# Optimization experiments

Measured on AMD Instinct MI355X. Metric: run time of the kernel, lower is better.

## Reference

```python
import jax, jax.numpy as jnp
import numpy as np

DIM = 128; NH = 4; WS = 7; SS = 3
ZP, HP, WP = 14, 56, 56
NMLP = 512; EPS = 1e-5
N = WS ** 3  # tokens per window (343)


def _ln(x, g, b):
    m = x.mean(-1, keepdims=True)
    v = x.var(-1, keepdims=True)
    return (x - m) / jnp.sqrt(v + EPS) * g + b


def _rel_index():
    # static relative-position index for a cubic (WS,WS,WS) window
    c = np.stack(np.meshgrid(np.arange(WS), np.arange(WS), np.arange(WS), indexing='ij')).reshape(3, -1)
    rel = (c[:, :, None] - c[:, None, :]).transpose(1, 2, 0) + (WS - 1)
    rel[..., 0] *= (2 * WS - 1) ** 2
    rel[..., 1] *= (2 * WS - 1)
    return rel.sum(-1).reshape(-1)  # [N*N]


def _attn_mask():
    # static shifted-window attention mask, [nW, N, N]
    img = np.zeros((ZP, HP, WP), np.float32)
    cnt = 0
    sl = (slice(0, -WS), slice(-WS, -SS), slice(-SS, None))
    for z in sl:
        for h in sl:
            for w in sl:
                img[z, h, w] = cnt
                cnt += 1
    m = img.reshape(ZP // WS, WS, HP // WS, WS, WP // WS, WS)
    m = m.transpose(0, 2, 4, 1, 3, 5).reshape(-1, N)
    d = m[:, None, :] - m[:, :, None]
    return np.where(d != 0, np.float32(-100.0), np.float32(0.0))


_REL_IDX = jnp.asarray(_rel_index())
_MASK = jnp.asarray(_attn_mask())


def setup_inputs() -> dict:
    key = jax.random.key(0)
    ks = jax.random.split(key, 8)
    return {
        'x': jax.random.normal(ks[0], (2, ZP, HP, WP, DIM), jnp.float32),
        'norm1_g': jnp.ones((DIM,), jnp.float32),
        'norm1_b': jnp.zeros((DIM,), jnp.float32),
        'qkv_w': jax.random.normal(ks[1], (DIM, 3 * DIM), jnp.float32) * 0.02,
        'qkv_b': jnp.zeros((3 * DIM,), jnp.float32),
        'rel_table': jax.random.normal(ks[2], ((2 * WS - 1) ** 3, NH), jnp.float32) * 0.02,
        'proj_w': jax.random.normal(ks[3], (DIM, DIM), jnp.float32) * 0.02,
        'proj_b': jnp.zeros((DIM,), jnp.float32),
        'norm2_g': jnp.ones((DIM,), jnp.float32),
        'norm2_b': jnp.zeros((DIM,), jnp.float32),
        'fc1_w': jax.random.normal(ks[4], (DIM, NMLP), jnp.float32) * 0.02,
        'fc1_b': jnp.zeros((NMLP,), jnp.float32),
        'fc2_w': jax.random.normal(ks[5], (NMLP, DIM), jnp.float32) * 0.02,
        'fc2_b': jnp.zeros((DIM,), jnp.float32),
    }


def reference(x, norm1_g, norm1_b, qkv_w, qkv_b, rel_table, proj_w, proj_b,
              norm2_g, norm2_b, fc1_w, fc1_b, fc2_w, fc2_b):
    B, Z, H, W, C = x.shape
    hd = C // NH
    scale = hd ** -0.5
    shortcut = x
    xn = _ln(x, norm1_g, norm1_b)
    # cyclic shift
    xs = jnp.roll(xn, (-SS, -SS, -SS), axis=(1, 2, 3))
    # window partition -> [B*nW, N, C]
    xw = xs.reshape(B, Z // WS, WS, H // WS, WS, W // WS, WS, C)
    xw = xw.transpose(0, 1, 3, 5, 2, 4, 6, 7).reshape(-1, N, C)
    qkv = (xw @ qkv_w + qkv_b).reshape(-1, N, 3, NH, hd).transpose(2, 0, 3, 1, 4)
    q, k, v = qkv[0], qkv[1], qkv[2]  # [Bn, NH, N, hd]
    attn = jnp.einsum('bhnd,bhmd->bhnm', q * scale, k)
    bias = rel_table[_REL_IDX].reshape(N, N, NH).transpose(2, 0, 1)  # [NH, N, N]
    attn = attn + bias[None]
    nW = _MASK.shape[0]
    attn = attn.reshape(B, nW, NH, N, N) + _MASK[None, :, None]
    attn = jax.nn.softmax(attn.reshape(-1, NH, N, N), axis=-1)
    out = jnp.einsum('bhnm,bhmd->bhnd', attn, v)
    out = out.transpose(0, 2, 1, 3).reshape(-1, N, C)
    out = out @ proj_w + proj_b
    # window reverse -> [B, Z, H, W, C]
    out = out.reshape(B, Z // WS, H // WS, W // WS, WS, WS, WS, C)
    out = out.transpose(0, 1, 4, 2, 5, 3, 6, 7).reshape(B, Z, H, W, C)
    out = jnp.roll(out, (SS, SS, SS), axis=(1, 2, 3))
    x1 = shortcut + out
    y = _ln(x1, norm2_g, norm2_b)
    y = jax.nn.gelu(y @ fc1_w + fc1_b, approximate=False) @ fc2_w + fc2_b
    return x1 + y
```

## Files before the change

### kernel.cpp

```cpp
#include <hip/hip_runtime.h>


typedef __attribute__((ext_vector_type(8))) _Float16 half8;
typedef __attribute__((ext_vector_type(4))) _Float16 half4;
typedef __attribute__((ext_vector_type(4))) float floatx4;

#define DEV static __device__ __forceinline__

DEV floatx4 MFMA(half8 a, half8 b, floatx4 c) {
  return __builtin_amdgcn_mfma_f32_16x16x32_f16(a, b, c, 0, 0, 0);
}
DEV floatx4 MFMA16(half4 a, half4 b, floatx4 c) {
  return __builtin_amdgcn_mfma_f32_16x16x16f16(a, b, c, 0, 0, 0);
}

DEV float gelu_f(float v) {
  return v / (1.f + __expf(-1.702f * v));
}

DEV void f4arr(float4 v, float o[4]) {
  o[0] = v.x; o[1] = v.y; o[2] = v.z; o[3] = v.w;
}

DEV void stage_load(half8 pf[8], const _Float16* src, int rst, int tid) {
#pragma unroll
  for (int it = 0; it < 8; ++it) {
    int e = it * 256 + tid;
    int row = e >> 4, seg = e & 15;
    pf[it] = *(const half8*)&src[(size_t)row * rst + seg * 8];
  }
}
DEV void stage_store(_Float16* wb, const half8 pf[8], int tid) {
#pragma unroll
  for (int it = 0; it < 8; ++it) {
    int e = it * 256 + tid;
    int row = e >> 4, seg = e & 15;
    *(half8*)&wb[row * 136 + seg * 8] = pf[it];
  }
}
DEV void stage_tile(_Float16* wb, const _Float16* src, int rst, int tid) {
  half8 pf[8];
  stage_load(pf, src, rst, tid);
  stage_store(wb, pf, tid);
}

__global__ __launch_bounds__(256) void k_prep(
    const float* __restrict__ rel, _Float16* __restrict__ biasH,
    const float* __restrict__ w1, const float* __restrict__ w2,
    const float* __restrict__ wq, const float* __restrict__ wp,
    _Float16* __restrict__ w1h, _Float16* __restrict__ w2h,
    _Float16* __restrict__ wqh, _Float16* __restrict__ wph) {
  int gid = blockIdx.x * 256 + threadIdx.x;
  if (gid < 495616) {
    int reg = gid & 3, quad = (gid >> 2) & 3, ml = (gid >> 4) & 15;
    int u = gid >> 8;
    int nt = u % 22; u /= 22;
    int rt = u % 22; int h = u / 22;
    int q = rt * 16 + ml, kv = nt * 16 + quad * 4 + reg;
    float val = -30000.f;
    if (q < 343 && kv < 343) {
      int lzi = q / 49, ri = q - lzi * 49, lhi = ri / 7, lwi = ri - lhi * 7;
      int lzj = kv / 49, rj = kv - lzj * 49, lhj = rj / 7, lwj = rj - lhj * 7;
      int idx = (lzi - lzj + 6) * 169 + (lhi - lhj + 6) * 13 + (lwi - lwj + 6);
      val = rel[idx * 4 + h];
    }
    biasH[gid] = (_Float16)val;
    return;
  }
  int i = gid - 495616;
  if (i < 65536) {
    int n = i >> 7, k = i & 127;
    w1h[i] = (_Float16)w1[k * 512 + n];
  } else if (i < 131072) {
    int j = i - 65536; int n = j >> 9, k = j & 511;
    w2h[j] = (_Float16)w2[k * 128 + n];
  } else if (i < 180224) {
    int j = i - 131072; int n = j >> 7, k = j & 127;
    wqh[j] = (_Float16)wq[k * 384 + n];
  } else if (i < 196608) {
    int j = i - 180224; int n = j >> 7, k = j & 127;
    wph[j] = (_Float16)wp[k * 128 + n];
  }
}

__global__ __launch_bounds__(256) void k_ln_qkv(
    const float* __restrict__ x, const float* __restrict__ g1,
    const float* __restrict__ b1, const _Float16* __restrict__ wqh,
    const float* __restrict__ bq, _Float16* __restrict__ qkv) {
  __shared__ __align__(16) _Float16 wb[128 * 136];
  const int tid = threadIdx.x, lane = tid & 63, wid = tid >> 6;
  const int ml = lane & 15, quad = lane >> 4;
  const int task = blockIdx.x * 4 + wid;
  const int w = task / 11, pr = task - (task / 11) * 11;
  const int b_ = w >> 7, r = w & 127;
  const int wz = r >> 6, wh = (r >> 3) & 7, ww = r & 7;

  half8 a0[4], a1[4];
#pragma unroll
  for (int hf = 0; hf < 2; ++hf) {
    int t = pr * 32 + hf * 16 + ml; if (t > 342) t = 342;
    int lz = t / 49, rr = t - lz * 49, lh = rr / 7, lw = rr - lh * 7;
    int oz = wz * 7 + lz + 3; if (oz >= 14) oz -= 14;
    int oh = wh * 7 + lh + 3; if (oh >= 56) oh -= 56;
    int ow = ww * 7 + lw + 3; if (ow >= 56) ow -= 56;
    const float* xp = x + ((((b_ * 14 + oz) * 56 + oh) * 56 + ow) << 7);
    float xv[32];
    float s = 0.f, ss = 0.f;
#pragma unroll
    for (int ks = 0; ks < 4; ++ks) {
      float4 p0 = *(const float4*)(xp + ks * 32 + quad * 8);
      float4 p1 = *(const float4*)(xp + ks * 32 + quad * 8 + 4);
      xv[ks * 8 + 0] = p0.x; xv[ks * 8 + 1] = p0.y; xv[ks * 8 + 2] = p0.z; xv[ks * 8 + 3] = p0.w;
      xv[ks * 8 + 4] = p1.x; xv[ks * 8 + 5] = p1.y; xv[ks * 8 + 6] = p1.z; xv[ks * 8 + 7] = p1.w;
      s += (p0.x + p0.y) + (p0.z + p0.w) + (p1.x + p1.y) + (p1.z + p1.w);
      ss += (p0.x * p0.x + p0.y * p0.y) + (p0.z * p0.z + p0.w * p0.w) +
            (p1.x * p1.x + p1.y * p1.y) + (p1.z * p1.z + p1.w * p1.w);
    }
    s += __shfl_xor(s, 16); s += __shfl_xor(s, 32);
    ss += __shfl_xor(ss, 16); ss += __shfl_xor(ss, 32);
    float mean = s * 0.0078125f;
    float rstd = rsqrtf(ss * 0.0078125f - mean * mean + 1e-5f);
#pragma unroll
    for (int ks = 0; ks < 4; ++ks) {
      int k0 = ks * 32 + quad * 8;
      float4 gg0 = *(const float4*)(g1 + k0), gg1 = *(const float4*)(g1 + k0 + 4);
      float4 bb0 = *(const float4*)(b1 + k0), bb1 = *(const float4*)(b1 + k0 + 4);
      half8 a;
      a[0] = (_Float16)((xv[ks * 8 + 0] - mean) * rstd * gg0.x + bb0.x);
      a[1] = (_Float16)((xv[ks * 8 + 1] - mean) * rstd * gg0.y + bb0.y);
      a[2] = (_Float16)((xv[ks * 8 + 2] - mean) * rstd * gg0.z + bb0.z);
      a[3] = (_Float16)((xv[ks * 8 + 3] - mean) * rstd * gg0.w + bb0.w);
      a[4] = (_Float16)((xv[ks * 8 + 4] - mean) * rstd * gg1.x + bb1.x);
      a[5] = (_Float16)((xv[ks * 8 + 5] - mean) * rstd * gg1.y + bb1.y);
      a[6] = (_Float16)((xv[ks * 8 + 6] - mean) * rstd * gg1.z + bb1.z);
      a[7] = (_Float16)((xv[ks * 8 + 7] - mean) * rstd * gg1.w + bb1.w);
      if (hf == 0) a0[ks] = a; else a1[ks] = a;
    }
  }

  const int t0 = pr * 32 + ml;
  const int t1 = t0 + 16;
  _Float16* q0 = qkv + ((size_t)w * 343 + t0) * 384;
  _Float16* q1 = qkv + ((size_t)w * 343 + (t1 < 343 ? t1 : 342)) * 384;

  for (int c = 0; c < 3; ++c) {
    __syncthreads();
    stage_tile(wb, wqh + (size_t)c * 128 * 128, 128, tid);
    __syncthreads();
    for (int ntl = 0; ntl < 8; ++ntl) {
      floatx4 acc0 = {0.f, 0.f, 0.f, 0.f}, acc1 = {0.f, 0.f, 0.f, 0.f};
#pragma unroll
      for (int ks = 0; ks < 4; ++ks) {
        half8 bb = *(const half8*)&wb[(ntl * 16 + ml) * 136 + ks * 32 + quad * 8];
        acc0 = MFMA(bb, a0[ks], acc0);
        acc1 = MFMA(bb, a1[ks], acc1);
      }
      const int colb = c * 128 + ntl * 16 + quad * 4;
      float qb[4]; f4arr(*(const float4*)&bq[colb], qb);
      half4 s0, s1;
#pragma unroll
      for (int reg = 0; reg < 4; ++reg) {
        s0[reg] = (_Float16)(acc0[reg] + qb[reg]);
        s1[reg] = (_Float16)(acc1[reg] + qb[reg]);
      }
      *(half4*)&q0[colb] = s0;
      if (t1 < 343) *(half4*)&q1[colb] = s1;
    }
  }
}

__global__ __launch_bounds__(512, 2) void k_attn(const _Float16* __restrict__ qkv,
                                                 const _Float16* __restrict__ biasH,
                                                 _Float16* __restrict__ aout) {
  __shared__ __align__(16) _Float16 kl[352 * 40];
  __shared__ __align__(16) _Float16 vt[32 * 364];
  __shared__ __align__(16) _Float16 pen[27 * 360];
  __shared__ __align__(4) unsigned char region[352];
  const int tid = threadIdx.x;
  const int w = blockIdx.x >> 2, head = blockIdx.x & 3;
  const int r = w & 127;
  const int wz = r >> 6, wh = (r >> 3) & 7, ww = r & 7;
  const bool fz = (wz == 1), fh = (wh == 7), fw = (ww == 7);

  for (int t = tid; t < 352; t += 512) {
    int rg = 255;
    if (t < 343) {
      int lz = t / 49, rr = t - lz * 49, lh = rr / 7, lw = rr - lh * 7;
      int rz = fz ? (lz < 4 ? 1 : 2) : 0;
      int rh2 = fh ? (lh < 4 ? 1 : 2) : 0;
      int rw2 = fw ? (lw < 4 ? 1 : 2) : 0;
      rg = rz * 9 + rh2 * 3 + rw2;
    }
    region[t] = (unsigned char)rg;
  }
  for (int e = tid; e < 27 * 352; e += 512) {
    int rg = e / 352, t = e - rg * 352;
    int rt_ = 255;
    if (t < 343) {
      int lz = t / 49, rr = t - lz * 49, lh = rr / 7, lw = rr - lh * 7;
      int rz = fz ? (lz < 4 ? 1 : 2) : 0;
      int rh2 = fh ? (lh < 4 ? 1 : 2) : 0;
      int rw2 = fw ? (lw < 4 ? 1 : 2) : 0;
      rt_ = rz * 9 + rh2 * 3 + rw2;
    }
    pen[rg * 360 + t] = (rt_ == rg) ? (_Float16)0.f : (_Float16)(-30000.f);
  }
  const _Float16* qkvw = qkv + (size_t)w * 343 * 384;
  for (int e = tid; e < 352 * 4; e += 512) {
    int t = e >> 2, d8 = (e & 3) * 8;
    half8 v;
    if (t < 343) {
      v = *(const half8*)&qkvw[t * 384 + 128 + head * 32 + d8];
    } else {
#pragma unroll
      for (int j = 0; j < 8; ++j) v[j] = (_Float16)0.f;
    }
    *(half8*)&kl[t * 40 + d8] = v;
  }
  for (int e = tid; e < 343 * 4; e += 512) {
    int t = e >> 2, d8 = (e & 3) * 8;
    half8 v = *(const half8*)&qkvw[t * 384 + 256 + head * 32 + d8];
#pragma unroll
    for (int j = 0; j < 8; ++j) vt[(d8 + j) * 364 + t] = v[j];
  }
  for (int e = tid; e < 9 * 32; e += 512) {
    int t = 343 + (e >> 5), d = e & 31;
    vt[d * 364 + t] = (_Float16)0.f;
  }
  __syncthreads();

  const int lane = tid & 63, wid = tid >> 6;
  const int ml = lane & 15, quad = lane >> 4;
  const float scale = 0.17677669529663687f;

  for (int rt = wid; rt < 22; rt += 8) {
    const int row0 = rt * 16;
    int qrow = row0 + ml; if (qrow > 342) qrow = 342;
    half8 bq8 = *(const half8*)&qkvw[qrow * 384 + head * 32 + quad * 8];
    const int rq = region[qrow];
    const _Float16* penr = &pen[rq * 360 + quad * 4];
    const _Float16* bb = &biasH[(size_t)((head * 22 + rt) * 22) * 256 + ml * 16 + quad * 4];

    floatx4 o0 = {0.f, 0.f, 0.f, 0.f}, o1 = {0.f, 0.f, 0.f, 0.f};
    floatx4 sm4 = {0.f, 0.f, 0.f, 0.f};
#pragma unroll
    for (int g = 0; g < 3; ++g) {
      const int G = (g < 2) ? 8 : 6;
      const int nb = g * 8;
      half4 bp[8];
      floatx4 S[8];
#pragma unroll
      for (int k = 0; k < 8; ++k) if (k < G) {
        half4 b4 = *(const half4*)&bb[(nb + k) * 256];
        half4 p4 = *(const half4*)&penr[(nb + k) * 16];
        bp[k] = b4 + p4;
      }
#pragma unroll
      for (int k = 0; k < 8; ++k) if (k < G) {
        half8 ak = *(const half8*)&kl[((nb + k) * 16 + ml) * 40 + quad * 8];
        S[k] = MFMA(ak, bq8, (floatx4){0.f, 0.f, 0.f, 0.f});
      }
#pragma unroll
      for (int k = 0; k < 8; ++k) if (k < G) {
        half4 p;
#pragma unroll
        for (int reg = 0; reg < 4; ++reg) {
          float v = fmaf(S[k][reg], scale, (float)bp[k][reg]);
          float e = __expf(v);
          sm4[reg] += e;
          p[reg] = (_Float16)e;
        }
        half4 va0 = *(const half4*)&vt[ml * 364 + (nb + k) * 16 + quad * 4];
        half4 va1 = *(const half4*)&vt[(16 + ml) * 364 + (nb + k) * 16 + quad * 4];
        o0 = MFMA16(va0, p, o0);
        o1 = MFMA16(va1, p, o1);
      }
    }
    float sm = (sm4[0] + sm4[1]) + (sm4[2] + sm4[3]);
    sm += __shfl_xor(sm, 16);
    sm += __shfl_xor(sm, 32);

    const int orow = row0 + ml;
    if (orow < 343) {
      float inv = 1.f / sm;
      _Float16* op = aout + ((size_t)w * 343 + orow) * 128 + head * 32;
      half4 s0, s1;
#pragma unroll
      for (int reg = 0; reg < 4; ++reg) {
        s0[reg] = (_Float16)(o0[reg] * inv);
        s1[reg] = (_Float16)(o1[reg] * inv);
      }
      *(half4*)&op[quad * 4] = s0;
      *(half4*)&op[16 + quad * 4] = s1;
    }
  }
}

__global__ __launch_bounds__(256, 2) void k_pm(
    const _Float16* __restrict__ aout, const _Float16* __restrict__ wph,
    const float* __restrict__ bp, const float* __restrict__ x,
    const float* __restrict__ g2, const float* __restrict__ nb2,
    const _Float16* __restrict__ w1h, const float* __restrict__ bfc1,
    const _Float16* __restrict__ w2h, const float* __restrict__ bfc2,
    float* __restrict__ out) {
  __shared__ __align__(16) _Float16 hc[4][16 * 136];
  __shared__ __align__(16) _Float16 wb[128 * 136];
  const int tid = threadIdx.x, lane = tid & 63, wid = tid >> 6;
  const int ml = lane & 15, quad = lane >> 4;
  const int task = blockIdx.x * 4 + wid;
  const int w = task / 22, tk = task - (task / 22) * 22;
  const int b_ = w >> 7, r = w & 127;
  const int wz = r >> 6, wh = (r >> 3) & 7, ww = r & 7;
  const _Float16* ap = aout + (size_t)w * 343 * 128;
  _Float16* hw = &hc[wid][0];

  half8 pf[8];
  stage_load(pf, wph, 128, tid);

  int ra = tk * 16 + ml; if (ra > 342) ra = 342;
  half8 a0[4];
#pragma unroll
  for (int ks = 0; ks < 4; ++ks)
    a0[ks] = *(const half8*)&ap[ra * 128 + ks * 32 + quad * 8];

  int tok;
  {
    int t = tk * 16 + ml;
    if (t < 343) {
      int lz = t / 49, rr = t - lz * 49, lh = rr / 7, lw = rr - lh * 7;
      int oz = wz * 7 + lz + 3; if (oz >= 14) oz -= 14;
      int oh = wh * 7 + lh + 3; if (oh >= 56) oh -= 56;
      int ow = ww * 7 + lw + 3; if (ow >= 56) ow -= 56;
      tok = ((b_ * 14 + oz) * 56 + oh) * 56 + ow;
    } else {
      tok = -1;
    }
  }
  stage_store(wb, pf, tid);
  __syncthreads();
  stage_load(pf, w1h, 128, tid);

  floatx4 px[8];
  for (int nt = 0; nt < 8; ++nt) {
    floatx4 acc = {0.f, 0.f, 0.f, 0.f};
#pragma unroll
    for (int ks = 0; ks < 4; ++ks) {
      half8 bb = *(const half8*)&wb[(nt * 16 + ml) * 136 + ks * 32 + quad * 8];
      acc = MFMA(bb, a0[ks], acc);
    }
    const int colb = nt * 16 + quad * 4;
    float pb4[4]; f4arr(*(const float4*)&bp[colb], pb4);
    float xr[4] = {0.f, 0.f, 0.f, 0.f};
    if (tok >= 0) f4arr(*(const float4*)&x[(size_t)tok * 128 + colb], xr);
#pragma unroll
    for (int reg = 0; reg < 4; ++reg)
      px[nt][reg] = acc[reg] + pb4[reg] + xr[reg];
  }

  float mean, rstd;
  {
    float s = 0.f, ss = 0.f;
#pragma unroll
    for (int nt = 0; nt < 8; ++nt)
#pragma unroll
      for (int reg = 0; reg < 4; ++reg) {
        float v = px[nt][reg];
        s += v; ss += v * v;
      }
    s += __shfl_xor(s, 16); s += __shfl_xor(s, 32);
    ss += __shfl_xor(ss, 16); ss += __shfl_xor(ss, 32);
    mean = s * 0.0078125f;
    rstd = rsqrtf(ss * 0.0078125f - mean * mean + 1e-5f);
  }

  for (int nt = 0; nt < 8; ++nt) {
    const int colb = nt * 16 + quad * 4;
    float g4[4], nb4[4];
    f4arr(*(const float4*)&g2[colb], g4);
    f4arr(*(const float4*)&nb2[colb], nb4);
    half4 h;
#pragma unroll
    for (int reg = 0; reg < 4; ++reg)
      h[reg] = (_Float16)((px[nt][reg] - mean) * rstd * g4[reg] + nb4[reg]);
    *(half4*)&hw[ml * 136 + colb] = h;
  }
  half8 ay[4];
#pragma unroll
  for (int ks = 0; ks < 4; ++ks)
    ay[ks] = *(const half8*)&hw[ml * 136 + ks * 32 + quad * 8];

  floatx4 acc2[8];
#pragma unroll
  for (int nt = 0; nt < 8; ++nt) acc2[nt] = (floatx4){0.f, 0.f, 0.f, 0.f};

  for (int ch = 0; ch < 4; ++ch) {
    __syncthreads();
    stage_store(wb, pf, tid);
    __syncthreads();
    stage_load(pf, w2h + (size_t)ch * 128, 512, tid);
    for (int nt = 0; nt < 8; ++nt) {
      floatx4 f0 = {0.f, 0.f, 0.f, 0.f};
#pragma unroll
      for (int ks = 0; ks < 4; ++ks) {
        half8 bb = *(const half8*)&wb[(nt * 16 + ml) * 136 + ks * 32 + quad * 8];
        f0 = MFMA(bb, ay[ks], f0);
      }
      const int colb = nt * 16 + quad * 4;
      float fb4[4]; f4arr(*(const float4*)&bfc1[ch * 128 + colb], fb4);
      half4 h0;
#pragma unroll
      for (int reg = 0; reg < 4; ++reg)
        h0[reg] = (_Float16)gelu_f(f0[reg] + fb4[reg]);
      *(half4*)&hw[ml * 136 + colb] = h0;
    }
    __syncthreads();
    stage_store(wb, pf, tid);
    __syncthreads();
    if (ch < 3) stage_load(pf, w1h + (size_t)(ch + 1) * 128 * 128, 128, tid);
#pragma unroll
    for (int ks = 0; ks < 4; ++ks) {
      half8 A0 = *(const half8*)&hw[ml * 136 + ks * 32 + quad * 8];
#pragma unroll
      for (int nt = 0; nt < 8; ++nt) {
        half8 bb = *(const half8*)&wb[(nt * 16 + ml) * 136 + ks * 32 + quad * 8];
        acc2[nt] = MFMA(bb, A0, acc2[nt]);
      }
    }
  }

  if (tok >= 0) {
    for (int nt = 0; nt < 8; ++nt) {
      const int colb = nt * 16 + quad * 4;
      float fb4[4]; f4arr(*(const float4*)&bfc2[colb], fb4);
      float4 o;
      o.x = px[nt][0] + acc2[nt][0] + fb4[0];
      o.y = px[nt][1] + acc2[nt][1] + fb4[1];
      o.z = px[nt][2] + acc2[nt][2] + fb4[2];
      o.w = px[nt][3] + acc2[nt][3] + fb4[3];
      *(float4*)&out[(size_t)tok * 128 + colb] = o;
    }
  }
}

extern "C" void kernel_launch(void* const* d_in, const int* in_sizes, int n_in,
                              void* d_out, int out_size, void* d_ws, size_t ws_size,
                              hipStream_t stream) {
  (void)in_sizes; (void)n_in; (void)out_size; (void)ws_size;
  const float* x   = (const float*)d_in[0];
  const float* g1  = (const float*)d_in[1];
  const float* b1  = (const float*)d_in[2];
  const float* wq  = (const float*)d_in[3];
  const float* bq  = (const float*)d_in[4];
  const float* rel = (const float*)d_in[5];
  const float* wp  = (const float*)d_in[6];
  const float* bp  = (const float*)d_in[7];
  const float* g2  = (const float*)d_in[8];
  const float* b2_ = (const float*)d_in[9];
  const float* w1  = (const float*)d_in[10];
  const float* bf1 = (const float*)d_in[11];
  const float* w2  = (const float*)d_in[12];
  const float* bf2 = (const float*)d_in[13];

  char* ws = (char*)d_ws;
  _Float16* qkv   = (_Float16*)(ws);
  _Float16* aout  = (_Float16*)(ws + 67436544);
  _Float16* biasH = (_Float16*)(ws + 89915392);
  _Float16* w1h   = (_Float16*)(ws + 91897856);
  _Float16* w2h   = (_Float16*)(ws + 92028928);
  _Float16* wqh   = (_Float16*)(ws + 92160000);
  _Float16* wph   = (_Float16*)(ws + 92258304);
  float*    out   = (float*)d_out;

  hipLaunchKernelGGL(k_prep,   dim3(2704), dim3(256), 0, stream,
                     rel, biasH, w1, w2, wq, wp, w1h, w2h, wqh, wph);
  hipLaunchKernelGGL(k_ln_qkv, dim3(704),  dim3(256), 0, stream, x, g1, b1, wqh, bq, qkv);
  hipLaunchKernelGGL(k_attn,   dim3(1024), dim3(512), 0, stream, qkv, biasH, aout);
  hipLaunchKernelGGL(k_pm,     dim3(1408), dim3(256), 0, stream,
                     aout, wph, bp, x, g2, b2_, w1h, bf1, w2h, bf2, out);
}
```

Before: 280.5 us.

## Read MLP and projection weights directly from global memory instead of LDS staging

The post-attention kernel no longer stages the proj, fc1 and fc2 weight tiles into a shared LDS buffer with block-wide barriers. Each wave now loads its MFMA B-operands straight from global memory, relying on the L2/L1 caches because every block reads the same weights. This removes the per-chunk __syncthreads pairs and the large LDS allocation, which may also allow more blocks per CU. The trade-off is many more global/cache loads per MFMA and more exposed load latency, since there is no longer any prefetch overlapping the weight loads with compute.

```diff
diff --git a/kernel.cpp b/kernel.cpp
--- a/kernel.cpp
+++ b/kernel.cpp
@@ -304,7 +304,6 @@
     const _Float16* __restrict__ w2h, const float* __restrict__ bfc2,
     float* __restrict__ out) {
   __shared__ __align__(16) _Float16 hc[4][16 * 136];
-  __shared__ __align__(16) _Float16 wb[128 * 136];
   const int tid = threadIdx.x, lane = tid & 63, wid = tid >> 6;
   const int ml = lane & 15, quad = lane >> 4;
   const int task = blockIdx.x * 4 + wid;
@@ -313,9 +312,6 @@
   const int wz = r >> 6, wh = (r >> 3) & 7, ww = r & 7;
   const _Float16* ap = aout + (size_t)w * 343 * 128;
   _Float16* hw = &hc[wid][0];
-
-  half8 pf[8];
-  stage_load(pf, wph, 128, tid);
 
   int ra = tk * 16 + ml; if (ra > 342) ra = 342;
   half8 a0[4];
@@ -336,18 +332,20 @@
       tok = -1;
     }
   }
-  stage_store(wb, pf, tid);
-  __syncthreads();
-  stage_load(pf, w1h, 128, tid);
-
+
+  const _Float16* wpr = wph + (size_t)ml * 128 + quad * 8;
   floatx4 px[8];
   for (int nt = 0; nt < 8; ++nt) {
+    const _Float16* wr = wpr + (size_t)nt * 16 * 128;
+    half8 b0 = *(const half8*)&wr[0];
+    half8 b1 = *(const half8*)&wr[32];
+    half8 b2 = *(const half8*)&wr[64];
+    half8 b3 = *(const half8*)&wr[96];
     floatx4 acc = {0.f, 0.f, 0.f, 0.f};
-#pragma unroll
-    for (int ks = 0; ks < 4; ++ks) {
-      half8 bb = *(const half8*)&wb[(nt * 16 + ml) * 136 + ks * 32 + quad * 8];
-      acc = MFMA(bb, a0[ks], acc);
-    }
+    acc = MFMA(b0, a0[0], acc);
+    acc = MFMA(b1, a0[1], acc);
+    acc = MFMA(b2, a0[2], acc);
+    acc = MFMA(b3, a0[3], acc);
     const int colb = nt * 16 + quad * 4;
     float pb4[4]; f4arr(*(const float4*)&bp[colb], pb4);
     float xr[4] = {0.f, 0.f, 0.f, 0.f};
@@ -393,18 +391,21 @@
 #pragma unroll
   for (int nt = 0; nt < 8; ++nt) acc2[nt] = (floatx4){0.f, 0.f, 0.f, 0.f};
 
+  const _Float16* w1r = w1h + (size_t)ml * 128 + quad * 8;
+  const _Float16* w2r = w2h + (size_t)ml * 512 + quad * 8;
+
   for (int ch = 0; ch < 4; ++ch) {
-    __syncthreads();
-    stage_store(wb, pf, tid);
-    __syncthreads();
-    stage_load(pf, w2h + (size_t)ch * 128, 512, tid);
     for (int nt = 0; nt < 8; ++nt) {
+      const _Float16* wr = w1r + (size_t)(ch * 128 + nt * 16) * 128;
+      half8 b0 = *(const half8*)&wr[0];
+      half8 b1 = *(const half8*)&wr[32];
+      half8 b2 = *(const half8*)&wr[64];
+      half8 b3 = *(const half8*)&wr[96];
       floatx4 f0 = {0.f, 0.f, 0.f, 0.f};
-#pragma unroll
-      for (int ks = 0; ks < 4; ++ks) {
-        half8 bb = *(const half8*)&wb[(nt * 16 + ml) * 136 + ks * 32 + quad * 8];
-        f0 = MFMA(bb, ay[ks], f0);
-      }
+      f0 = MFMA(b0, ay[0], f0);
+      f0 = MFMA(b1, ay[1], f0);
+      f0 = MFMA(b2, ay[2], f0);
+      f0 = MFMA(b3, ay[3], f0);
       const int colb = nt * 16 + quad * 4;
       float fb4[4]; f4arr(*(const float4*)&bfc1[ch * 128 + colb], fb4);
       half4 h0;
@@ -413,16 +414,12 @@
         h0[reg] = (_Float16)gelu_f(f0[reg] + fb4[reg]);
       *(half4*)&hw[ml * 136 + colb] = h0;
     }
-    __syncthreads();
-    stage_store(wb, pf, tid);
-    __syncthreads();
-    if (ch < 3) stage_load(pf, w1h + (size_t)(ch + 1) * 128 * 128, 128, tid);
 #pragma unroll
     for (int ks = 0; ks < 4; ++ks) {
       half8 A0 = *(const half8*)&hw[ml * 136 + ks * 32 + quad * 8];
 #pragma unroll
       for (int nt = 0; nt < 8; ++nt) {
-        half8 bb = *(const half8*)&wb[(nt * 16 + ml) * 136 + ks * 32 + quad * 8];
+        half8 bb = *(const half8*)&w2r[(size_t)nt * 16 * 512 + ch * 128 + ks * 32];
         acc2[nt] = MFMA(bb, A0, acc2[nt]);
       }
     }
```

New measurement: 418.7 us. +49.3%, slower.
